# Kernel optimization log

Measured on AMD Instinct MI355X. Metric: run time of the kernel, lower is better.

## Reference

```python
import jax, jax.numpy as jnp
import numpy as np

BS, L, NPH, NQ, H = 64, 512, 16, 16, 1024
EPS = 1e-5

def _ln(x, g, b):
    m = jnp.mean(x, axis=-1, keepdims=True)
    v = jnp.mean((x - m) ** 2, axis=-1, keepdims=True)
    return (x - m) * jax.lax.rsqrt(v + EPS) * g + b

def setup_inputs() -> dict:
    key = jax.random.key(0)
    ks = jax.random.split(key, 24)
    s = 0.02
    inp = {
        "lang_context_feat": jax.random.normal(ks[0], (BS, L, H), jnp.float32),
        "lang_query_feat": jax.random.normal(ks[1], (BS, NPH, H), jnp.float32),
        "mask_query_context": jax.random.randint(ks[2], (BS, NPH, L), 0, 2).astype(bool),
        "query_embed": jax.random.normal(ks[3], (NQ, 2 * H), jnp.float32) * s,
        # linear1/2/3: hidden -> hidden (stored [in, out])
        "W1": jax.random.normal(ks[4], (H, H), jnp.float32) * s, "b1": jnp.zeros((H,), jnp.float32),
        "W2": jax.random.normal(ks[5], (H, H), jnp.float32) * s, "b2": jnp.zeros((H,), jnp.float32),
        "W3": jax.random.normal(ks[6], (H, H), jnp.float32) * s, "b3": jnp.zeros((H,), jnp.float32),
        # context_out: Linear(h,h) + LayerNorm(h)
        "Wc": jax.random.normal(ks[7], (H, H), jnp.float32) * s, "bc": jnp.zeros((H,), jnp.float32),
        "gc": jnp.ones((H,), jnp.float32), "betac": jnp.zeros((H,), jnp.float32),
        # fuse_encoder_query: Linear(2h,h)+LN+ReLU+Dropout(eval)+Linear(h,h)+LN+ReLU
        "Wf1": jax.random.normal(ks[8], (2 * H, H), jnp.float32) * s, "bf1": jnp.zeros((H,), jnp.float32),
        "gf1": jnp.ones((H,), jnp.float32), "betaf1": jnp.zeros((H,), jnp.float32),
        "Wf2": jax.random.normal(ks[9], (H, H), jnp.float32) * s, "bf2": jnp.zeros((H,), jnp.float32),
        "gf2": jnp.ones((H,), jnp.float32), "betaf2": jnp.zeros((H,), jnp.float32),
    }
    return inp

def reference(lang_context_feat, lang_query_feat, mask_query_context,
              query_embed, W1, b1, W2, b2, W3, b3,
              Wc, bc, gc, betac,
              Wf1, bf1, gf1, betaf1, Wf2, bf2, gf2, betaf2):
    # single-query attention: k from first context token, q/v from all tokens
    k = lang_context_feat[:, 0:1, :] @ W1 + b1          # [bs,1,h]
    q = lang_context_feat @ W2 + b2                     # [bs,L,h]
    v = lang_context_feat @ W3 + b3                     # [bs,L,h]
    att = jnp.einsum("bih,blh->bil", k, q)             # [bs,1,L]
    att = jnp.broadcast_to(att, mask_query_context.shape)  # [bs,n_ph,L]
    att = jnp.where(mask_query_context, -jnp.inf, att)
    p = jax.nn.softmax(att, axis=-1)                    # [bs,n_ph,L]
    ctx = jnp.einsum("bpl,blh->bph", p, v)             # [bs,n_ph,h]
    ctx = _ln(ctx @ Wc + bc, gc, betac)
    ctx = lang_context_feat[:, None, 0, :] + ctx        # residual with first token
    x = jnp.concatenate([ctx, lang_query_feat], axis=-1)   # [bs,n_ph,2h]
    x = jax.nn.relu(_ln(x @ Wf1 + bf1, gf1, betaf1))        # dropout: eval mode (identity)
    x = jax.nn.relu(_ln(x @ Wf2 + bf2, gf2, betaf2))        # [bs,n_ph,h]
    # repeat(1,1,1,2) on last dim == tile [x, x]
    pq = jnp.concatenate([x, x], axis=-1)[:, :, None, :]    # [bs,n_ph,1,2h]
    pq = pq + query_embed[None, None, :, :]                 # [bs,n_ph,n_q,2h]
    pq = pq.reshape(pq.shape[0], -1, 2 * H).transpose(1, 0, 2)  # [n_ph*n_q,bs,2h]
    return pq[..., :H], pq[..., H:]
```

## Files before the change

### kernel.cpp

```cpp
#include <hip/hip_runtime.h>

typedef __bf16 bf16;
typedef __bf16 bf16x8 __attribute__((ext_vector_type(8)));
typedef __bf16 bf16x4 __attribute__((ext_vector_type(4)));
typedef float f32x4 __attribute__((ext_vector_type(4)));

#define BSZ 64
#define LCTX 512
#define NPH 16
#define NQ 16
#define HD 1024

__global__ __launch_bounds__(256) void prep_kernel(const float* __restrict__ W3,
                                                   const float* __restrict__ Wc,
                                                   const float* __restrict__ Wf1,
                                                   const float* __restrict__ Wf2,
                                                   const float* __restrict__ lq,
                                                   bf16* __restrict__ W3t, bf16* __restrict__ Wct,
                                                   bf16* __restrict__ Wf1t, bf16* __restrict__ Wf2t,
                                                   bf16* __restrict__ X) {
    __shared__ float tile[32][33];
    int blk = blockIdx.x, t = threadIdx.x;
    if (blk < 5120) {
        const float* W; bf16* Wt; int K, N, i;
        if (blk < 1024)      { W = W3;  Wt = W3t;  K = 1024; N = 1024; i = blk; }
        else if (blk < 2048) { W = Wc;  Wt = Wct;  K = 1024; N = 1024; i = blk - 1024; }
        else if (blk < 3072) { W = Wf2; Wt = Wf2t; K = 1024; N = 1024; i = blk - 2048; }
        else                 { W = Wf1; Wt = Wf1t; K = 2048; N = 1024; i = blk - 3072; }
        int k0 = (i >> 5) * 32, n0 = (i & 31) * 32;
        int c = t & 31, r = t >> 5;
#pragma unroll
        for (int j = 0; j < 4; j++)
            tile[r + j * 8][c] = W[(size_t)(k0 + r + j * 8) * N + n0 + c];
        __syncthreads();
#pragma unroll
        for (int j = 0; j < 4; j++)
            Wt[(size_t)(n0 + r + j * 8) * K + k0 + c] = (bf16)tile[c][r + j * 8];
    } else {
        int i = (blk - 5120) * 256 + t;
        float4 v = ((const float4*)lq)[i];
        int row = i >> 8, h4 = i & 255;
        bf16x4 o = {(bf16)v.x, (bf16)v.y, (bf16)v.z, (bf16)v.w};
        *(bf16x4*)(X + (size_t)row * 2048 + 1024 + h4 * 4) = o;
    }
}

__global__ __launch_bounds__(256) void kpart_kernel(const float* __restrict__ x,
                                                    const float* __restrict__ W1,
                                                    float* __restrict__ partial) {
    __shared__ float xs[64][68];
    __shared__ float ws[64][64];
    int n0 = blockIdx.x * 64, k0 = blockIdx.y * 64;
    int t = threadIdx.x;
#pragma unroll
    for (int i = 0; i < 4; i++) {
        int f = t + i * 256;
        int b = f >> 4, c = f & 15;
        *(float4*)&xs[b][c * 4] =
            *(const float4*)(x + (size_t)b * LCTX * HD + k0 + c * 4);
    }
#pragma unroll
    for (int i = 0; i < 4; i++) {
        int f = t + i * 256;
        int r = f >> 4, c = f & 15;
        *(float4*)&ws[r][c * 4] =
            *(const float4*)(W1 + (size_t)(k0 + r) * 1024 + n0 + c * 4);
    }
    __syncthreads();
    int tb = t >> 4, tc = t & 15;
    int b0 = tb * 4;
    float acc[4][4] = {};
    for (int kk = 0; kk < 64; kk += 4) {
        float4 w0 = *(const float4*)&ws[kk + 0][tc * 4];
        float4 w1 = *(const float4*)&ws[kk + 1][tc * 4];
        float4 w2 = *(const float4*)&ws[kk + 2][tc * 4];
        float4 w3 = *(const float4*)&ws[kk + 3][tc * 4];
        float4 xv[4];
#pragma unroll
        for (int bi = 0; bi < 4; bi++) xv[bi] = *(const float4*)&xs[b0 + bi][kk];
#pragma unroll
        for (int bi = 0; bi < 4; bi++) {
            acc[bi][0] += xv[bi].x * w0.x + xv[bi].y * w1.x + xv[bi].z * w2.x + xv[bi].w * w3.x;
            acc[bi][1] += xv[bi].x * w0.y + xv[bi].y * w1.y + xv[bi].z * w2.y + xv[bi].w * w3.y;
            acc[bi][2] += xv[bi].x * w0.z + xv[bi].y * w1.z + xv[bi].z * w2.z + xv[bi].w * w3.z;
            acc[bi][3] += xv[bi].x * w0.w + xv[bi].y * w1.w + xv[bi].z * w2.w + xv[bi].w * w3.w;
        }
    }
    float* pout = partial + ((size_t)blockIdx.y * 64 + b0) * 1024 + n0 + tc * 4;
#pragma unroll
    for (int bi = 0; bi < 4; bi++) {
        float4 o = make_float4(acc[bi][0], acc[bi][1], acc[bi][2], acc[bi][3]);
        *(float4*)(pout + (size_t)bi * 1024) = o;
    }
}

__global__ __launch_bounds__(256) void kreduce_kernel(const float* __restrict__ partial,
                                                      const float* __restrict__ b1,
                                                      float* __restrict__ kout) {
    int b = blockIdx.x, t = threadIdx.x;
    float4 acc = ((const float4*)b1)[t];
#pragma unroll
    for (int kt = 0; kt < 16; kt++) {
        float4 v = ((const float4*)(partial + ((size_t)kt * 64 + b) * 1024))[t];
        acc.x += v.x; acc.y += v.y; acc.z += v.z; acc.w += v.w;
    }
    ((float4*)(kout + (size_t)b * 1024))[t] = acc;
}

__global__ __launch_bounds__(256) void mmat_kernel(const float* __restrict__ kin,
                                                   const float* __restrict__ W2,
                                                   float* __restrict__ mout) {
    __shared__ float ks[1024];
    int b = blockIdx.x, i0 = blockIdx.y * 64, t = threadIdx.x;
    *(float4*)&ks[t * 4] = ((const float4*)(kin + (size_t)b * 1024))[t];
    __syncthreads();
    int wave = t >> 6, lane = t & 63;
    for (int rr = 0; rr < 16; rr++) {
        int i = i0 + wave * 16 + rr;
        const float* wrow = W2 + (size_t)i * 1024;
        float s = 0.f;
#pragma unroll
        for (int j = 0; j < 4; j++) {
            float4 wv = ((const float4*)wrow)[lane + j * 64];
            const float4 kv = *(const float4*)&ks[(lane + j * 64) * 4];
            s += wv.x * kv.x + wv.y * kv.y + wv.z * kv.z + wv.w * kv.w;
        }
        for (int off = 32; off; off >>= 1) s += __shfl_xor(s, off, 64);
        if (lane == 0) mout[(size_t)b * 1024 + i] = s;
    }
}

__global__ __launch_bounds__(256) void att_kernel(const float* __restrict__ x,
                                                  const float* __restrict__ m,
                                                  float* __restrict__ att) {
    __shared__ float ms[1024];
    int b = blockIdx.x, l0 = blockIdx.y * 64, t = threadIdx.x;
    *(float4*)&ms[t * 4] = ((const float4*)(m + (size_t)b * 1024))[t];
    __syncthreads();
    int wave = t >> 6, lane = t & 63;
    for (int rr = 0; rr < 16; rr++) {
        int l = l0 + wave * 16 + rr;
        const float* xr = x + ((size_t)b * LCTX + l) * HD;
        float s = 0.f;
#pragma unroll
        for (int j = 0; j < 4; j++) {
            float4 xv = ((const float4*)xr)[lane + j * 64];
            const float4 mv = *(const float4*)&ms[(lane + j * 64) * 4];
            s += xv.x * mv.x + xv.y * mv.y + xv.z * mv.z + xv.w * mv.w;
        }
        for (int off = 32; off; off >>= 1) s += __shfl_xor(s, off, 64);
        if (lane == 0) att[(size_t)b * LCTX + l] = s;
    }
}

__global__ __launch_bounds__(256) void softmax_kernel(const float* __restrict__ att,
                                                      const unsigned char* __restrict__ mask,
                                                      float* __restrict__ p) {
    __shared__ float red1[8], red2[8];
    __shared__ int sstr;
    int bp = blockIdx.x, b = bp >> 4, t = threadIdx.x;
    if (t == 0) sstr = 4;
    __syncthreads();
    if (t < 128 && ((const unsigned int*)mask)[t] > 1u) sstr = 1;
    __syncthreads();
    int stride = sstr;
    size_t base = (size_t)bp * LCTX;
    bool mk0 = mask[(base + t) * (size_t)stride] != 0;
    bool mk1 = mask[(base + t + 256) * (size_t)stride] != 0;
    float a0 = mk0 ? -1e30f : att[(size_t)b * LCTX + t];
    float a1 = mk1 ? -1e30f : att[(size_t)b * LCTX + t + 256];
    float mx = fmaxf(a0, a1);
    for (int off = 32; off; off >>= 1) mx = fmaxf(mx, __shfl_xor(mx, off, 64));
    int wave = t >> 6, lane = t & 63;
    if (lane == 0) red1[wave] = mx;
    __syncthreads();
    mx = fmaxf(fmaxf(red1[0], red1[1]), fmaxf(red1[2], red1[3]));
    float e0 = mk0 ? 0.f : expf(a0 - mx);
    float e1 = mk1 ? 0.f : expf(a1 - mx);
    float s = e0 + e1;
    for (int off = 32; off; off >>= 1) s += __shfl_xor(s, off, 64);
    if (lane == 0) red2[wave] = s;
    __syncthreads();
    s = red2[0] + red2[1] + red2[2] + red2[3];
    float inv = 1.f / s;
    p[base + t] = e0 * inv;
    p[base + t + 256] = e1 * inv;
}

__global__ __launch_bounds__(256) void y_kernel(const float* __restrict__ x,
                                                const float* __restrict__ p,
                                                bf16* __restrict__ y) {
    __shared__ float ps[16][512];
    int b = blockIdx.x, c0 = blockIdx.y * 256, t = threadIdx.x;
    const float4* pp = (const float4*)(p + (size_t)b * 16 * 512);
    float4* psv = (float4*)ps;
    for (int i = t; i < 2048; i += 256) psv[i] = pp[i];
    __syncthreads();
    float acc[16] = {};
    const float* xb = x + (size_t)b * LCTX * HD + c0 + t;
    for (int l = 0; l < 512; l++) {
        float xv = xb[(size_t)l * HD];
#pragma unroll
        for (int q = 0; q < 16; q++) acc[q] += ps[q][l] * xv;
    }
#pragma unroll
    for (int q = 0; q < 16; q++)
        y[((size_t)(b * 16 + q)) * HD + c0 + t] = (bf16)acc[q];
}

__device__ __forceinline__ void gl16(const bf16* g, bf16* l) {
    __builtin_amdgcn_global_load_lds((const __attribute__((address_space(1))) void*)g,
                                     (__attribute__((address_space(3))) void*)l, 16, 0, 0);
}
__device__ __forceinline__ bf16x8 ldsfrag(const bf16* base, int row, int kb) {
    return *(const bf16x8*)(base + row * 64 + ((kb ^ (row & 7)) << 3));
}

template <bool OUT_BF16>
__global__ __launch_bounds__(256) void gemm_kernel(const bf16* __restrict__ A, int lda,
                                                   const bf16* __restrict__ Bt, int ldb,
                                                   const float* __restrict__ bias,
                                                   void* __restrict__ Cv, int ldc, int K) {
    __shared__ bf16 sA[2][4096];
    __shared__ bf16 sB[2][4096];
    int tid = threadIdx.x;
    int wave = tid >> 6, lane = tid & 63;
    int m0 = blockIdx.x * 64, n0 = blockIdx.y * 64;
    int wr = (wave >> 1) * 32, wc = (wave & 1) * 32;
    int l16 = lane & 15, lhi = lane >> 4;

    int r0 = tid >> 3, kb = tid & 7;
    int r1 = r0 + 32;
    int sk0 = (kb ^ (r0 & 7)) << 3;
    int sk1 = (kb ^ (r1 & 7)) << 3;
    const bf16* A0 = A + (size_t)(m0 + r0) * lda + sk0;
    const bf16* A1 = A + (size_t)(m0 + r1) * lda + sk1;
    const bf16* B0 = Bt + (size_t)(n0 + r0) * ldb + sk0;
    const bf16* B1 = Bt + (size_t)(n0 + r1) * ldb + sk1;
    int wb0 = (wave * 64) * 8;
    int wb1 = (256 + wave * 64) * 8;

    f32x4 acc00 = {}, acc01 = {}, acc10 = {}, acc11 = {};

    int nt = K >> 6;
    gl16(A0, &sA[0][wb0]); gl16(A1, &sA[0][wb1]);
    gl16(B0, &sB[0][wb0]); gl16(B1, &sB[0][wb1]);
    asm volatile("s_waitcnt vmcnt(0)" ::: "memory");
    __syncthreads();
    int cur = 0;
    for (int tI = 0; tI < nt; ++tI) {
        if (tI + 1 < nt) {
            int ko = (tI + 1) << 6;
            gl16(A0 + ko, &sA[cur ^ 1][wb0]); gl16(A1 + ko, &sA[cur ^ 1][wb1]);
            gl16(B0 + ko, &sB[cur ^ 1][wb0]); gl16(B1 + ko, &sB[cur ^ 1][wb1]);
        }
        const bf16* a = sA[cur];
        const bf16* bt = sB[cur];
#pragma unroll
        for (int ks = 0; ks < 2; ks++) {
            int kbb = ks * 4 + lhi;
            bf16x8 a0 = ldsfrag(a, wr + l16, kbb);
            bf16x8 a1v = ldsfrag(a, wr + 16 + l16, kbb);
            bf16x8 b0v = ldsfrag(bt, wc + l16, kbb);
            bf16x8 b1v = ldsfrag(bt, wc + 16 + l16, kbb);
            acc00 = __builtin_amdgcn_mfma_f32_16x16x32_bf16(a0, b0v, acc00, 0, 0, 0);
            acc01 = __builtin_amdgcn_mfma_f32_16x16x32_bf16(a0, b1v, acc01, 0, 0, 0);
            acc10 = __builtin_amdgcn_mfma_f32_16x16x32_bf16(a1v, b0v, acc10, 0, 0, 0);
            acc11 = __builtin_amdgcn_mfma_f32_16x16x32_bf16(a1v, b1v, acc11, 0, 0, 0);
        }
        asm volatile("s_waitcnt vmcnt(0)" ::: "memory");
        __syncthreads();
        cur ^= 1;
    }
    f32x4 accs[2][2] = {{acc00, acc01}, {acc10, acc11}};
#pragma unroll
    for (int mi = 0; mi < 2; mi++)
#pragma unroll
        for (int ni = 0; ni < 2; ni++)
#pragma unroll
            for (int r = 0; r < 4; r++) {
                int row = m0 + wr + mi * 16 + lhi * 4 + r;
                int col = n0 + wc + ni * 16 + l16;
                float v = accs[mi][ni][r] + bias[col];
                if (OUT_BF16)
                    ((bf16*)Cv)[(size_t)row * ldc + col] = (bf16)v;
                else
                    ((float*)Cv)[(size_t)row * ldc + col] = v;
            }
}

template <int MODE>
__global__ __launch_bounds__(256) void ln_kernel(const float* __restrict__ C,
                                                 const float* __restrict__ g,
                                                 const float* __restrict__ beta,
                                                 const float* __restrict__ resid,
                                                 void* __restrict__ out) {
    __shared__ float r1[8], r2[8];
    int row = blockIdx.x, t = threadIdx.x;
    float4 v = ((const float4*)(C + (size_t)row * 1024))[t];
    float s = v.x + v.y + v.z + v.w;
    float s2 = v.x * v.x + v.y * v.y + v.z * v.z + v.w * v.w;
    for (int off = 32; off; off >>= 1) {
        s += __shfl_xor(s, off, 64);
        s2 += __shfl_xor(s2, off, 64);
    }
    int wave = t >> 6, lane = t & 63;
    if (lane == 0) { r1[wave] = s; r2[wave] = s2; }
    __syncthreads();
    float S = r1[0] + r1[1] + r1[2] + r1[3];
    float S2 = r2[0] + r2[1] + r2[2] + r2[3];
    float mean = S * (1.f / 1024.f);
    float var = S2 * (1.f / 1024.f) - mean * mean;
    float inv = rsqrtf(var + 1e-5f);
    float4 gv = ((const float4*)g)[t];
    float4 bv = ((const float4*)beta)[t];
    float o[4];
    o[0] = (v.x - mean) * inv * gv.x + bv.x;
    o[1] = (v.y - mean) * inv * gv.y + bv.y;
    o[2] = (v.z - mean) * inv * gv.z + bv.z;
    o[3] = (v.w - mean) * inv * gv.w + bv.w;
    if (MODE == 0) {
        int b = row >> 4;
        const float* x0 = resid + (size_t)b * LCTX * HD + t * 4;
        bf16x4 w = {(bf16)(o[0] + x0[0]), (bf16)(o[1] + x0[1]),
                    (bf16)(o[2] + x0[2]), (bf16)(o[3] + x0[3])};
        *(bf16x4*)((bf16*)out + (size_t)row * 2048 + t * 4) = w;
    } else {
        bf16x4 w = {(bf16)fmaxf(o[0], 0.f), (bf16)fmaxf(o[1], 0.f),
                    (bf16)fmaxf(o[2], 0.f), (bf16)fmaxf(o[3], 0.f)};
        *(bf16x4*)((bf16*)out + (size_t)row * 1024 + t * 4) = w;
    }
}

__global__ __launch_bounds__(256) void lnout_kernel(const float* __restrict__ C,
                                                    const float* __restrict__ g,
                                                    const float* __restrict__ beta,
                                                    const float* __restrict__ qe,
                                                    float* __restrict__ out) {
    __shared__ float r1[8], r2[8];
    int row = blockIdx.x, t = threadIdx.x;
    int b = row >> 4, pp = row & 15;
    float4 v = ((const float4*)(C + (size_t)row * 1024))[t];
    float s = v.x + v.y + v.z + v.w;
    float s2 = v.x * v.x + v.y * v.y + v.z * v.z + v.w * v.w;
    for (int off = 32; off; off >>= 1) {
        s += __shfl_xor(s, off, 64);
        s2 += __shfl_xor(s2, off, 64);
    }
    int wave = t >> 6, lane = t & 63;
    if (lane == 0) { r1[wave] = s; r2[wave] = s2; }
    __syncthreads();
    float S = r1[0] + r1[1] + r1[2] + r1[3];
    float S2 = r2[0] + r2[1] + r2[2] + r2[3];
    float mean = S * (1.f / 1024.f);
    float var = S2 * (1.f / 1024.f) - mean * mean;
    float inv = rsqrtf(var + 1e-5f);
    float4 gv = ((const float4*)g)[t];
    float4 bv = ((const float4*)beta)[t];
    float4 ov;
    ov.x = fmaxf((v.x - mean) * inv * gv.x + bv.x, 0.f);
    ov.y = fmaxf((v.y - mean) * inv * gv.y + bv.y, 0.f);
    ov.z = fmaxf((v.z - mean) * inv * gv.z + bv.z, 0.f);
    ov.w = fmaxf((v.w - mean) * inv * gv.w + bv.w, 0.f);
    float* out0 = out;
    float* out1 = out + (size_t)256 * 64 * 1024;
#pragma unroll
    for (int q = 0; q < 16; q++) {
        float4 q0 = ((const float4*)(qe + (size_t)q * 2048))[t];
        float4 q1 = ((const float4*)(qe + (size_t)q * 2048 + 1024))[t];
        size_t orow = ((size_t)(pp * 16 + q) * 64 + b) * 1024;
        float4 w0 = make_float4(ov.x + q0.x, ov.y + q0.y, ov.z + q0.z, ov.w + q0.w);
        float4 w1 = make_float4(ov.x + q1.x, ov.y + q1.y, ov.z + q1.z, ov.w + q1.w);
        ((float4*)(out0 + orow))[t] = w0;
        ((float4*)(out1 + orow))[t] = w1;
    }
}

extern "C" void kernel_launch(void* const* d_in, const int* in_sizes, int n_in,
                              void* d_out, int out_size, void* d_ws, size_t ws_size,
                              hipStream_t stream) {
    const float* x      = (const float*)d_in[0];
    const float* lq     = (const float*)d_in[1];
    const unsigned char* mask = (const unsigned char*)d_in[2];
    const float* qe     = (const float*)d_in[3];
    const float* W1     = (const float*)d_in[4];
    const float* b1     = (const float*)d_in[5];
    const float* W2     = (const float*)d_in[6];
    const float* W3     = (const float*)d_in[8];
    const float* b3     = (const float*)d_in[9];
    const float* Wc     = (const float*)d_in[10];
    const float* bc     = (const float*)d_in[11];
    const float* gc     = (const float*)d_in[12];
    const float* betac  = (const float*)d_in[13];
    const float* Wf1    = (const float*)d_in[14];
    const float* bf1    = (const float*)d_in[15];
    const float* gf1    = (const float*)d_in[16];
    const float* betaf1 = (const float*)d_in[17];
    const float* Wf2    = (const float*)d_in[18];
    const float* bf2    = (const float*)d_in[19];
    const float* gf2    = (const float*)d_in[20];
    const float* betaf2 = (const float*)d_in[21];

    char* ws = (char*)d_ws;
    const size_t MB = 1 << 20;
    bf16* W3t   = (bf16*)(ws + 0 * MB);
    bf16* Wct   = (bf16*)(ws + 2 * MB);
    bf16* Wf1t  = (bf16*)(ws + 4 * MB);
    bf16* Wf2t  = (bf16*)(ws + 8 * MB);
    bf16* X     = (bf16*)(ws + 10 * MB);
    float* kbuf = (float*)(ws + 14 * MB);
    float* mbuf = (float*)(ws + 14 * MB + 256 * 1024);
    float* attb = (float*)(ws + 14 * MB + 512 * 1024);
    float* pbuf = (float*)(ws + 15 * MB);
    bf16* ybuf  = (bf16*)(ws + 17 * MB);
    bf16* ctxp  = (bf16*)(ws + 19 * MB);
    float* Cbuf = (float*)(ws + 21 * MB);
    bf16* t1    = (bf16*)(ws + 25 * MB);
    float* kpartial = Cbuf;

    prep_kernel<<<6144, 256, 0, stream>>>(W3, Wc, Wf1, Wf2, lq, W3t, Wct, Wf1t, Wf2t, X);
    kpart_kernel<<<dim3(16, 16), 256, 0, stream>>>(x, W1, kpartial);
    kreduce_kernel<<<64, 256, 0, stream>>>(kpartial, b1, kbuf);
    mmat_kernel<<<dim3(64, 16), 256, 0, stream>>>(kbuf, W2, mbuf);
    att_kernel<<<dim3(64, 8), 256, 0, stream>>>(x, mbuf, attb);
    softmax_kernel<<<1024, 256, 0, stream>>>(attb, mask, pbuf);
    y_kernel<<<dim3(64, 4), 256, 0, stream>>>(x, pbuf, ybuf);
    gemm_kernel<true><<<dim3(16, 16), 256, 0, stream>>>(ybuf, 1024, W3t, 1024, b3,
                                                        ctxp, 1024, 1024);
    gemm_kernel<false><<<dim3(16, 16), 256, 0, stream>>>(ctxp, 1024, Wct, 1024, bc,
                                                         Cbuf, 1024, 1024);
    ln_kernel<0><<<1024, 256, 0, stream>>>(Cbuf, gc, betac, x, X);
    gemm_kernel<false><<<dim3(16, 16), 256, 0, stream>>>(X, 2048, Wf1t, 2048, bf1,
                                                         Cbuf, 1024, 2048);
    ln_kernel<1><<<1024, 256, 0, stream>>>(Cbuf, gf1, betaf1, nullptr, t1);
    gemm_kernel<false><<<dim3(16, 16), 256, 0, stream>>>(t1, 1024, Wf2t, 1024, bf2,
                                                         Cbuf, 1024, 1024);
    lnout_kernel<<<1024, 256, 0, stream>>>(Cbuf, gf2, betaf2, qe, (float*)d_out);
}
```

Baseline: 231.0 us.

## Fuse k-projection into prep, k-reduce into mmat, softmax into y kernel

Folds the kpart GEMM into the prep kernel as extra blocks, moves the k partial-sum reduction into the mmat kernel prologue, and fuses the softmax with the attention-weighted sum so probabilities stay in shared memory. The att kernel grid is doubled with fewer rows per block. This removes three launches and the round trip of the probability buffer through global memory. In exchange, softmax work is repeated by each of the 4 column blocks per batch, and prep's shared memory grows, which may lower its occupancy.

```diff
diff --git a/kernel.cpp b/kernel.cpp
--- a/kernel.cpp
+++ b/kernel.cpp
@@ -5,23 +5,33 @@
 typedef __bf16 bf16x4 __attribute__((ext_vector_type(4)));
 typedef float f32x4 __attribute__((ext_vector_type(4)));
 
-#define BSZ 64
 #define LCTX 512
-#define NPH 16
-#define NQ 16
 #define HD 1024
+
+__device__ __forceinline__ float wave_sum(float v) {
+    for (int off = 32; off; off >>= 1) v += __shfl_xor(v, off, 64);
+    return v;
+}
+__device__ __forceinline__ float wave_max(float v) {
+    for (int off = 32; off; off >>= 1) v = fmaxf(v, __shfl_xor(v, off, 64));
+    return v;
+}
 
 __global__ __launch_bounds__(256) void prep_kernel(const float* __restrict__ W3,
                                                    const float* __restrict__ Wc,
                                                    const float* __restrict__ Wf1,
                                                    const float* __restrict__ Wf2,
                                                    const float* __restrict__ lq,
+                                                   const float* __restrict__ x,
+                                                   const float* __restrict__ W1,
                                                    bf16* __restrict__ W3t, bf16* __restrict__ Wct,
                                                    bf16* __restrict__ Wf1t, bf16* __restrict__ Wf2t,
-                                                   bf16* __restrict__ X) {
-    __shared__ float tile[32][33];
+                                                   bf16* __restrict__ X,
+                                                   float* __restrict__ kpartial) {
+    __shared__ __align__(16) char smem[33792];
     int blk = blockIdx.x, t = threadIdx.x;
     if (blk < 5120) {
+        float (*tile)[33] = (float(*)[33])smem;
         const float* W; bf16* Wt; int K, N, i;
         if (blk < 1024)      { W = W3;  Wt = W3t;  K = 1024; N = 1024; i = blk; }
         else if (blk < 2048) { W = Wc;  Wt = Wct;  K = 1024; N = 1024; i = blk - 1024; }
@@ -36,83 +46,74 @@
 #pragma unroll
         for (int j = 0; j < 4; j++)
             Wt[(size_t)(n0 + r + j * 8) * K + k0 + c] = (bf16)tile[c][r + j * 8];
-    } else {
+    } else if (blk < 6144) {
         int i = (blk - 5120) * 256 + t;
         float4 v = ((const float4*)lq)[i];
         int row = i >> 8, h4 = i & 255;
         bf16x4 o = {(bf16)v.x, (bf16)v.y, (bf16)v.z, (bf16)v.w};
         *(bf16x4*)(X + (size_t)row * 2048 + 1024 + h4 * 4) = o;
-    }
-}
-
-__global__ __launch_bounds__(256) void kpart_kernel(const float* __restrict__ x,
-                                                    const float* __restrict__ W1,
-                                                    float* __restrict__ partial) {
-    __shared__ float xs[64][68];
-    __shared__ float ws[64][64];
-    int n0 = blockIdx.x * 64, k0 = blockIdx.y * 64;
-    int t = threadIdx.x;
-#pragma unroll
-    for (int i = 0; i < 4; i++) {
-        int f = t + i * 256;
-        int b = f >> 4, c = f & 15;
-        *(float4*)&xs[b][c * 4] =
-            *(const float4*)(x + (size_t)b * LCTX * HD + k0 + c * 4);
-    }
-#pragma unroll
-    for (int i = 0; i < 4; i++) {
-        int f = t + i * 256;
-        int r = f >> 4, c = f & 15;
-        *(float4*)&ws[r][c * 4] =
-            *(const float4*)(W1 + (size_t)(k0 + r) * 1024 + n0 + c * 4);
-    }
-    __syncthreads();
-    int tb = t >> 4, tc = t & 15;
-    int b0 = tb * 4;
-    float acc[4][4] = {};
-    for (int kk = 0; kk < 64; kk += 4) {
-        float4 w0 = *(const float4*)&ws[kk + 0][tc * 4];
-        float4 w1 = *(const float4*)&ws[kk + 1][tc * 4];
-        float4 w2 = *(const float4*)&ws[kk + 2][tc * 4];
-        float4 w3 = *(const float4*)&ws[kk + 3][tc * 4];
-        float4 xv[4];
-#pragma unroll
-        for (int bi = 0; bi < 4; bi++) xv[bi] = *(const float4*)&xs[b0 + bi][kk];
-#pragma unroll
-        for (int bi = 0; bi < 4; bi++) {
-            acc[bi][0] += xv[bi].x * w0.x + xv[bi].y * w1.x + xv[bi].z * w2.x + xv[bi].w * w3.x;
-            acc[bi][1] += xv[bi].x * w0.y + xv[bi].y * w1.y + xv[bi].z * w2.y + xv[bi].w * w3.y;
-            acc[bi][2] += xv[bi].x * w0.z + xv[bi].y * w1.z + xv[bi].z * w2.z + xv[bi].w * w3.z;
-            acc[bi][3] += xv[bi].x * w0.w + xv[bi].y * w1.w + xv[bi].z * w2.w + xv[bi].w * w3.w;
-        }
-    }
-    float* pout = partial + ((size_t)blockIdx.y * 64 + b0) * 1024 + n0 + tc * 4;
-#pragma unroll
-    for (int bi = 0; bi < 4; bi++) {
-        float4 o = make_float4(acc[bi][0], acc[bi][1], acc[bi][2], acc[bi][3]);
-        *(float4*)(pout + (size_t)bi * 1024) = o;
-    }
-}
-
-__global__ __launch_bounds__(256) void kreduce_kernel(const float* __restrict__ partial,
-                                                      const float* __restrict__ b1,
-                                                      float* __restrict__ kout) {
-    int b = blockIdx.x, t = threadIdx.x;
-    float4 acc = ((const float4*)b1)[t];
-#pragma unroll
-    for (int kt = 0; kt < 16; kt++) {
-        float4 v = ((const float4*)(partial + ((size_t)kt * 64 + b) * 1024))[t];
-        acc.x += v.x; acc.y += v.y; acc.z += v.z; acc.w += v.w;
-    }
-    ((float4*)(kout + (size_t)b * 1024))[t] = acc;
-}
-
-__global__ __launch_bounds__(256) void mmat_kernel(const float* __restrict__ kin,
+    } else {
+        float (*xs)[68] = (float(*)[68])smem;
+        float (*wsm)[64] = (float(*)[64])(smem + 17408);
+        int kv = blk - 6144;
+        int n0 = (kv & 15) * 64, k0 = (kv >> 4) * 64;
+#pragma unroll
+        for (int i = 0; i < 4; i++) {
+            int f = t + i * 256;
+            int b = f >> 4, c = f & 15;
+            *(float4*)&xs[b][c * 4] =
+                *(const float4*)(x + (size_t)b * LCTX * HD + k0 + c * 4);
+        }
+#pragma unroll
+        for (int i = 0; i < 4; i++) {
+            int f = t + i * 256;
+            int r = f >> 4, c = f & 15;
+            *(float4*)&wsm[r][c * 4] =
+                *(const float4*)(W1 + (size_t)(k0 + r) * 1024 + n0 + c * 4);
+        }
+        __syncthreads();
+        int tb = t >> 4, tc = t & 15;
+        int b0 = tb * 4;
+        float acc[4][4] = {};
+        for (int kk = 0; kk < 64; kk += 4) {
+            float4 w0 = *(const float4*)&wsm[kk + 0][tc * 4];
+            float4 w1 = *(const float4*)&wsm[kk + 1][tc * 4];
+            float4 w2 = *(const float4*)&wsm[kk + 2][tc * 4];
+            float4 w3 = *(const float4*)&wsm[kk + 3][tc * 4];
+            float4 xv[4];
+#pragma unroll
+            for (int bi = 0; bi < 4; bi++) xv[bi] = *(const float4*)&xs[b0 + bi][kk];
+#pragma unroll
+            for (int bi = 0; bi < 4; bi++) {
+                acc[bi][0] += xv[bi].x * w0.x + xv[bi].y * w1.x + xv[bi].z * w2.x + xv[bi].w * w3.x;
+                acc[bi][1] += xv[bi].x * w0.y + xv[bi].y * w1.y + xv[bi].z * w2.y + xv[bi].w * w3.y;
+                acc[bi][2] += xv[bi].x * w0.z + xv[bi].y * w1.z + xv[bi].z * w2.z + xv[bi].w * w3.z;
+                acc[bi][3] += xv[bi].x * w0.w + xv[bi].y * w1.w + xv[bi].z * w2.w + xv[bi].w * w3.w;
+            }
+        }
+        float* pout = kpartial + ((size_t)(kv >> 4) * 64 + b0) * 1024 + n0 + tc * 4;
+#pragma unroll
+        for (int bi = 0; bi < 4; bi++)
+            *(float4*)(pout + (size_t)bi * 1024) =
+                make_float4(acc[bi][0], acc[bi][1], acc[bi][2], acc[bi][3]);
+    }
+}
+
+__global__ __launch_bounds__(256) void mmat_kernel(const float* __restrict__ partial,
+                                                   const float* __restrict__ b1,
                                                    const float* __restrict__ W2,
                                                    float* __restrict__ mout) {
     __shared__ float ks[1024];
     int b = blockIdx.x, i0 = blockIdx.y * 64, t = threadIdx.x;
-    *(float4*)&ks[t * 4] = ((const float4*)(kin + (size_t)b * 1024))[t];
+    {
+        float4 acc = ((const float4*)b1)[t];
+#pragma unroll
+        for (int kt = 0; kt < 16; kt++) {
+            float4 v = ((const float4*)(partial + ((size_t)kt * 64 + b) * 1024))[t];
+            acc.x += v.x; acc.y += v.y; acc.z += v.z; acc.w += v.w;
+        }
+        *(float4*)&ks[t * 4] = acc;
+    }
     __syncthreads();
     int wave = t >> 6, lane = t & 63;
     for (int rr = 0; rr < 16; rr++) {
@@ -125,7 +126,7 @@
             const float4 kv = *(const float4*)&ks[(lane + j * 64) * 4];
             s += wv.x * kv.x + wv.y * kv.y + wv.z * kv.z + wv.w * kv.w;
         }
-        for (int off = 32; off; off >>= 1) s += __shfl_xor(s, off, 64);
+        s = wave_sum(s);
         if (lane == 0) mout[(size_t)b * 1024 + i] = s;
     }
 }
@@ -134,12 +135,12 @@
                                                   const float* __restrict__ m,
                                                   float* __restrict__ att) {
     __shared__ float ms[1024];
-    int b = blockIdx.x, l0 = blockIdx.y * 64, t = threadIdx.x;
+    int b = blockIdx.x, l0 = blockIdx.y * 32, t = threadIdx.x;
     *(float4*)&ms[t * 4] = ((const float4*)(m + (size_t)b * 1024))[t];
     __syncthreads();
     int wave = t >> 6, lane = t & 63;
-    for (int rr = 0; rr < 16; rr++) {
-        int l = l0 + wave * 16 + rr;
+    for (int rr = 0; rr < 8; rr++) {
+        int l = l0 + wave * 8 + rr;
         const float* xr = x + ((size_t)b * LCTX + l) * HD;
         float s = 0.f;
 #pragma unroll
@@ -148,53 +149,52 @@
             const float4 mv = *(const float4*)&ms[(lane + j * 64) * 4];
             s += xv.x * mv.x + xv.y * mv.y + xv.z * mv.z + xv.w * mv.w;
         }
-        for (int off = 32; off; off >>= 1) s += __shfl_xor(s, off, 64);
+        s = wave_sum(s);
         if (lane == 0) att[(size_t)b * LCTX + l] = s;
     }
 }
 
-__global__ __launch_bounds__(256) void softmax_kernel(const float* __restrict__ att,
-                                                      const unsigned char* __restrict__ mask,
-                                                      float* __restrict__ p) {
-    __shared__ float red1[8], red2[8];
+__global__ __launch_bounds__(256) void ysm_kernel(const float* __restrict__ att,
+                                                  const unsigned char* __restrict__ mask,
+                                                  const float* __restrict__ x,
+                                                  bf16* __restrict__ y) {
+    __shared__ float ps[16][512];
+    __shared__ float att_s[512];
     __shared__ int sstr;
-    int bp = blockIdx.x, b = bp >> 4, t = threadIdx.x;
+    int b = blockIdx.x, c0 = blockIdx.y * 256, t = threadIdx.x;
+    int wave = t >> 6, lane = t & 63;
     if (t == 0) sstr = 4;
+    if (t < 128) ((float4*)att_s)[t] = ((const float4*)(att + (size_t)b * LCTX))[t];
     __syncthreads();
     if (t < 128 && ((const unsigned int*)mask)[t] > 1u) sstr = 1;
     __syncthreads();
     int stride = sstr;
-    size_t base = (size_t)bp * LCTX;
-    bool mk0 = mask[(base + t) * (size_t)stride] != 0;
-    bool mk1 = mask[(base + t + 256) * (size_t)stride] != 0;
-    float a0 = mk0 ? -1e30f : att[(size_t)b * LCTX + t];
-    float a1 = mk1 ? -1e30f : att[(size_t)b * LCTX + t + 256];
-    float mx = fmaxf(a0, a1);
-    for (int off = 32; off; off >>= 1) mx = fmaxf(mx, __shfl_xor(mx, off, 64));
-    int wave = t >> 6, lane = t & 63;
-    if (lane == 0) red1[wave] = mx;
-    __syncthreads();
-    mx = fmaxf(fmaxf(red1[0], red1[1]), fmaxf(red1[2], red1[3]));
-    float e0 = mk0 ? 0.f : expf(a0 - mx);
-    float e1 = mk1 ? 0.f : expf(a1 - mx);
-    float s = e0 + e1;
-    for (int off = 32; off; off >>= 1) s += __shfl_xor(s, off, 64);
-    if (lane == 0) red2[wave] = s;
-    __syncthreads();
-    s = red2[0] + red2[1] + red2[2] + red2[3];
-    float inv = 1.f / s;
-    p[base + t] = e0 * inv;
-    p[base + t + 256] = e1 * inv;
-}
-
-__global__ __launch_bounds__(256) void y_kernel(const float* __restrict__ x,
-                                                const float* __restrict__ p,
-                                                bf16* __restrict__ y) {
-    __shared__ float ps[16][512];
-    int b = blockIdx.x, c0 = blockIdx.y * 256, t = threadIdx.x;
-    const float4* pp = (const float4*)(p + (size_t)b * 16 * 512);
-    float4* psv = (float4*)ps;
-    for (int i = t; i < 2048; i += 256) psv[i] = pp[i];
+#pragma unroll
+    for (int q = 0; q < 4; q++) {
+        int pp = wave * 4 + q;
+        size_t mbase = ((size_t)(b * 16 + pp)) * LCTX;
+        float av[8];
+#pragma unroll
+        for (int j = 0; j < 8; j++) {
+            int l = lane + j * 64;
+            bool mk = mask[(mbase + l) * (size_t)stride] != 0;
+            av[j] = mk ? -1e30f : att_s[l];
+        }
+        float mx = av[0];
+#pragma unroll
+        for (int j = 1; j < 8; j++) mx = fmaxf(mx, av[j]);
+        mx = wave_max(mx);
+        float s = 0.f;
+#pragma unroll
+        for (int j = 0; j < 8; j++) {
+            av[j] = (av[j] <= -1e29f) ? 0.f : expf(av[j] - mx);
+            s += av[j];
+        }
+        s = wave_sum(s);
+        float inv = 1.f / s;
+#pragma unroll
+        for (int j = 0; j < 8; j++) ps[pp][lane + j * 64] = av[j] * inv;
+    }
     __syncthreads();
     float acc[16] = {};
     const float* xb = x + (size_t)b * LCTX * HD + c0 + t;
@@ -228,7 +228,6 @@
     int m0 = blockIdx.x * 64, n0 = blockIdx.y * 64;
     int wr = (wave >> 1) * 32, wc = (wave & 1) * 32;
     int l16 = lane & 15, lhi = lane >> 4;
-
     int r0 = tid >> 3, kb = tid & 7;
     int r1 = r0 + 32;
     int sk0 = (kb ^ (r0 & 7)) << 3;
@@ -300,10 +299,7 @@
     float4 v = ((const float4*)(C + (size_t)row * 1024))[t];
     float s = v.x + v.y + v.z + v.w;
     float s2 = v.x * v.x + v.y * v.y + v.z * v.z + v.w * v.w;
-    for (int off = 32; off; off >>= 1) {
-        s += __shfl_xor(s, off, 64);
-        s2 += __shfl_xor(s2, off, 64);
-    }
+    s = wave_sum(s); s2 = wave_sum(s2);
     int wave = t >> 6, lane = t & 63;
     if (lane == 0) { r1[wave] = s; r2[wave] = s2; }
     __syncthreads();
@@ -343,10 +339,7 @@
     float4 v = ((const float4*)(C + (size_t)row * 1024))[t];
     float s = v.x + v.y + v.z + v.w;
     float s2 = v.x * v.x + v.y * v.y + v.z * v.z + v.w * v.w;
-    for (int off = 32; off; off >>= 1) {
-        s += __shfl_xor(s, off, 64);
-        s2 += __shfl_xor(s2, off, 64);
-    }
+    s = wave_sum(s); s2 = wave_sum(s2);
     int wave = t >> 6, lane = t & 63;
     if (lane == 0) { r1[wave] = s; r2[wave] = s2; }
     __syncthreads();
@@ -369,10 +362,10 @@
         float4 q0 = ((const float4*)(qe + (size_t)q * 2048))[t];
         float4 q1 = ((const float4*)(qe + (size_t)q * 2048 + 1024))[t];
         size_t orow = ((size_t)(pp * 16 + q) * 64 + b) * 1024;
-        float4 w0 = make_float4(ov.x + q0.x, ov.y + q0.y, ov.z + q0.z, ov.w + q0.w);
-        float4 w1 = make_float4(ov.x + q1.x, ov.y + q1.y, ov.z + q1.z, ov.w + q1.w);
-        ((float4*)(out0 + orow))[t] = w0;
-        ((float4*)(out1 + orow))[t] = w1;
+        ((float4*)(out0 + orow))[t] =
+            make_float4(ov.x + q0.x, ov.y + q0.y, ov.z + q0.z, ov.w + q0.w);
+        ((float4*)(out1 + orow))[t] =
+            make_float4(ov.x + q1.x, ov.y + q1.y, ov.z + q1.z, ov.w + q1.w);
     }
 }
 
@@ -408,23 +401,19 @@
     bf16* Wf1t  = (bf16*)(ws + 4 * MB);
     bf16* Wf2t  = (bf16*)(ws + 8 * MB);
     bf16* X     = (bf16*)(ws + 10 * MB);
-    float* kbuf = (float*)(ws + 14 * MB);
     float* mbuf = (float*)(ws + 14 * MB + 256 * 1024);
     float* attb = (float*)(ws + 14 * MB + 512 * 1024);
-    float* pbuf = (float*)(ws + 15 * MB);
     bf16* ybuf  = (bf16*)(ws + 17 * MB);
     bf16* ctxp  = (bf16*)(ws + 19 * MB);
     float* Cbuf = (float*)(ws + 21 * MB);
     bf16* t1    = (bf16*)(ws + 25 * MB);
     float* kpartial = Cbuf;
 
-    prep_kernel<<<6144, 256, 0, stream>>>(W3, Wc, Wf1, Wf2, lq, W3t, Wct, Wf1t, Wf2t, X);
-    kpart_kernel<<<dim3(16, 16), 256, 0, stream>>>(x, W1, kpartial);
-    kreduce_kernel<<<64, 256, 0, stream>>>(kpartial, b1, kbuf);
-    mmat_kernel<<<dim3(64, 16), 256, 0, stream>>>(kbuf, W2, mbuf);
-    att_kernel<<<dim3(64, 8), 256, 0, stream>>>(x, mbuf, attb);
-    softmax_kernel<<<1024, 256, 0, stream>>>(attb, mask, pbuf);
-    y_kernel<<<dim3(64, 4), 256, 0, stream>>>(x, pbuf, ybuf);
+    prep_kernel<<<6400, 256, 0, stream>>>(W3, Wc, Wf1, Wf2, lq, x, W1,
+                                          W3t, Wct, Wf1t, Wf2t, X, kpartial);
+    mmat_kernel<<<dim3(64, 16), 256, 0, stream>>>(kpartial, b1, W2, mbuf);
+    att_kernel<<<dim3(64, 16), 256, 0, stream>>>(x, mbuf, attb);
+    ysm_kernel<<<dim3(64, 4), 256, 0, stream>>>(attb, mask, x, ybuf);
     gemm_kernel<true><<<dim3(16, 16), 256, 0, stream>>>(ybuf, 1024, W3t, 1024, b3,
                                                         ctxp, 1024, 1024);
     gemm_kernel<false><<<dim3(16, 16), 256, 0, stream>>>(ctxp, 1024, Wct, 1024, bc,
```

Result: slower. 257.7 us (+11.6%).
